# Kernel optimization log

Measured on AMD Instinct MI355X. Metric: run time of the kernel, lower is better.

## Reference

```python
import jax, jax.numpy as jnp
import numpy as np

NUM_EXPERTS = 8
HIDDEN = 2048
INTER = 4096
TOKENS = 8192  # divisible by NUM_EXPERTS


def setup_inputs() -> dict:
    key = jax.random.key(0)
    k1, k2, k3 = jax.random.split(key, 3)
    hidden_states = jax.random.normal(k1, (TOKENS, HIDDEN), dtype=jnp.float32)
    gate_up_proj = jax.random.normal(k2, (NUM_EXPERTS, HIDDEN, 2 * INTER), dtype=jnp.float32) * 0.02
    down_proj = jax.random.normal(k3, (NUM_EXPERTS, INTER, HIDDEN), dtype=jnp.float32) * 0.02
    return {"hidden_states": hidden_states, "gate_up_proj": gate_up_proj, "down_proj": down_proj}


def reference(hidden_states, gate_up_proj, down_proj):
    E, H = gate_up_proj.shape[0], gate_up_proj.shape[1]
    x = hidden_states.reshape(E, -1, H)                      # (E, T/E, H)
    gate_up = jnp.einsum('eth,ehf->etf', x, gate_up_proj)    # (E, T/E, 2I)
    gate, up = jnp.split(gate_up, 2, axis=-1)
    acted = up * jax.nn.silu(gate)                           # (E, T/E, I)
    out = jnp.einsum('eti,eih->eth', acted, down_proj)       # (E, T/E, H)
    return out.reshape(-1, H)
```

## Files before the change

kernel.cpp:

```cpp
#include <hip/hip_runtime.h>


#define E_   8
#define H_   2048
#define I_   4096
#define T_   8192
#define TPE  1024

typedef __bf16 bf16x8 __attribute__((ext_vector_type(8)));
typedef float  f32x4  __attribute__((ext_vector_type(4)));

__device__ __forceinline__ unsigned short f2bf(float f) {
  union { float f; unsigned int u; } v; v.f = f;
  unsigned int u = v.u;
  u += 0x7FFFu + ((u >> 16) & 1u);
  return (unsigned short)(u >> 16);
}

__device__ __forceinline__ void async16(const void* g, void* l) {
  __builtin_amdgcn_global_load_lds(
      (__attribute__((address_space(1))) void*)(g),
      (__attribute__((address_space(3))) void*)(l), 16, 0, 0);
}

#define SB0()      __builtin_amdgcn_sched_barrier(0)
#define BAR()      __builtin_amdgcn_s_barrier()
#define WAITLGKM() asm volatile("s_waitcnt lgkmcnt(0)" ::: "memory")
#define WAITVM(n)  asm volatile("s_waitcnt vmcnt(" #n ")" ::: "memory")

__global__ void convert_bf16(const float* __restrict__ src,
                             unsigned short* __restrict__ dst, long n) {
  long i = ((long)blockIdx.x * blockDim.x + threadIdx.x) * 4;
  const long stride = (long)gridDim.x * blockDim.x * 4;
  for (; i < n; i += stride) {
    const float4 v = *(const float4*)&src[i];
    ushort4 o;
    o.x = f2bf(v.x); o.y = f2bf(v.y); o.z = f2bf(v.z); o.w = f2bf(v.w);
    *(ushort4*)&dst[i] = o;
  }
}

template <int K, int NBN, int LDB, bool SILU>
__global__ __launch_bounds__(512, 2)
void gemm_fused(const unsigned short* __restrict__ Aall,
                const float* __restrict__ Ball,
                void* __restrict__ Cout,
                long sA, long sB, long sC) {
  extern __shared__ char smem[];
  constexpr int NT = K / 64;
  static_assert(NT % 2 == 0, "NT must be even for the x2 unroll");

  const int tid  = threadIdx.x;
  const int wave = tid >> 6;
  const int lane = tid & 63;
  const int lr   = lane & 15;
  const int lq   = lane >> 4;
  const int wid_m = wave >> 2;
  const int wid_n = wave & 3;

  const int nwg = gridDim.x;
  const int bid = blockIdx.x;
  const int wg  = (bid & 7) * (nwg >> 3) + (bid >> 3);
  const int mb  = wg & 3;
  const int tmp = wg >> 2;
  const int nb  = tmp % NBN;
  const int e   = tmp / NBN;

  const unsigned short* A = Aall + (long)e * sA + (long)(mb * 256) * K;
  const float*          B = Ball + (long)e * sB;

  const int stl  = tid >> 3;
  const int scol = ((tid & 7) ^ (stl & 7)) * 8;

  auto stageA = [&](int bi, int q, int kt) {
    const long col = (long)kt * 64 + scol;
    char* l0 = smem + bi * 32768 + q * 16384 + wave * 1024;
    async16(A + (long)(q * 64 + stl) * K + col,        l0);
    async16(A + (long)(128 + q * 64 + stl) * K + col,  l0 + 8192);
  };

  int cbase;
  if (SILU) {
    cbase = nb * 128 + (lane >> 5) * 64 + (lane & 15) * 4
          + (((lane >> 4) & 1) ? I_ : 0);
  } else {
    cbase = nb * 256 + lane * 4;
  }
  const float* Bq = B + cbase;

  f32x4 bvA[8], bvB[8];

  auto LOADB = [&](auto& bv, int kt) {
    const long kbase = (long)kt * 64 + wave * 8;
#pragma unroll
    for (int i = 0; i < 8; ++i)
      bv[i] = *(const f32x4*)&Bq[(kbase + i) * (long)LDB];
  };
  auto WRITEB = [&](int bo, auto& bv) {
    char* LBw = smem + 65536 + bo * 32768 + ((wave ^ (lane & 7)) * 16);
#pragma unroll
    for (int j = 0; j < 4; ++j) {
      bf16x8 pk;
#pragma unroll
      for (int i = 0; i < 8; ++i) pk[i] = (__bf16)bv[i][j];
      *(bf16x8*)(LBw + (64 * j + lane) * 128) = pk;
    }
  };

  const int ax0 = ((0 + lq) ^ (lr & 7)) * 16;
  const int ax1 = ((4 + lq) ^ (lr & 7)) * 16;

  f32x4 acc[8][4];
#pragma unroll
  for (int m = 0; m < 8; ++m)
#pragma unroll
    for (int n = 0; n < 4; ++n) acc[m][n] = (f32x4)0.0f;

  const int t1p = (NT > 1) ? 1 : 0;
  LOADB(bvA, 0);
  stageA(0, 0, 0);
  stageA(0, 1, 0);
  SB0();
  WAITVM(4); SB0();
  WRITEB(0, bvA);
  WAITLGKM(); SB0();
  stageA(1, 0, t1p); SB0();
  LOADB(bvB, t1p); SB0();
  stageA(1, 1, t1p); SB0();
  WAITVM(12); SB0();
  BAR();

  auto body = [&](int t, auto& bvW, auto& bvL) {
    const int cur = t & 1;
    const int bo  = cur ^ 1;
    const char* LA = smem + cur * 32768;
    const char* LB = smem + 65536 + cur * 32768;
    const int t2v = (t + 2 < NT) ? t + 2 : NT - 1;

    bf16x8 a[4][2], b0[2][2], b1[2][2];

#pragma unroll
    for (int mf = 0; mf < 4; ++mf) {
      const int st = wid_m * 64 + mf * 16 + lr;
      a[mf][0] = *(const bf16x8*)(LA + st * 128 + ax0);
      a[mf][1] = *(const bf16x8*)(LA + st * 128 + ax1);
    }
#pragma unroll
    for (int nf = 0; nf < 2; ++nf) {
      const int st = wid_n * 32 + nf * 16 + lr;
      b0[nf][0] = *(const bf16x8*)(LB + st * 128 + ax0);
      b0[nf][1] = *(const bf16x8*)(LB + st * 128 + ax1);
    }
    SB0();
    BAR();
    WAITLGKM(); SB0();
    __builtin_amdgcn_s_setprio(1);
#pragma unroll
    for (int mf = 0; mf < 4; ++mf)
#pragma unroll
      for (int nf = 0; nf < 2; ++nf) {
        acc[mf][nf] = __builtin_amdgcn_mfma_f32_16x16x32_bf16(a[mf][0], b0[nf][0], acc[mf][nf], 0, 0, 0);
        acc[mf][nf] = __builtin_amdgcn_mfma_f32_16x16x32_bf16(a[mf][1], b0[nf][1], acc[mf][nf], 0, 0, 0);
      }
    __builtin_amdgcn_s_setprio(0);
    BAR();

#pragma unroll
    for (int nf = 0; nf < 2; ++nf) {
      const int st = 128 + wid_n * 32 + nf * 16 + lr;
      b1[nf][0] = *(const bf16x8*)(LB + st * 128 + ax0);
      b1[nf][1] = *(const bf16x8*)(LB + st * 128 + ax1);
    }
    stageA(cur, 0, t2v);
    SB0();
    BAR();
    WAITLGKM(); SB0();
    __builtin_amdgcn_s_setprio(1);
#pragma unroll
    for (int mf = 0; mf < 4; ++mf)
#pragma unroll
      for (int nf = 0; nf < 2; ++nf) {
        acc[mf][2 + nf] = __builtin_amdgcn_mfma_f32_16x16x32_bf16(a[mf][0], b1[nf][0], acc[mf][2 + nf], 0, 0, 0);
        acc[mf][2 + nf] = __builtin_amdgcn_mfma_f32_16x16x32_bf16(a[mf][1], b1[nf][1], acc[mf][2 + nf], 0, 0, 0);
      }
    __builtin_amdgcn_s_setprio(0);
    BAR();

#pragma unroll
    for (int mf = 0; mf < 4; ++mf) {
      const int st = 128 + wid_m * 64 + mf * 16 + lr;
      a[mf][0] = *(const bf16x8*)(LA + st * 128 + ax0);
      a[mf][1] = *(const bf16x8*)(LA + st * 128 + ax1);
    }
    SB0();
    WAITVM(4); SB0();
    WRITEB(bo, bvW);
    LOADB(bvL, t2v);
    SB0();
    BAR();
    WAITLGKM(); SB0();
    __builtin_amdgcn_s_setprio(1);
#pragma unroll
    for (int mf = 0; mf < 4; ++mf)
#pragma unroll
      for (int nf = 0; nf < 2; ++nf) {
        acc[4 + mf][2 + nf] = __builtin_amdgcn_mfma_f32_16x16x32_bf16(a[mf][0], b1[nf][0], acc[4 + mf][2 + nf], 0, 0, 0);
        acc[4 + mf][2 + nf] = __builtin_amdgcn_mfma_f32_16x16x32_bf16(a[mf][1], b1[nf][1], acc[4 + mf][2 + nf], 0, 0, 0);
      }
    __builtin_amdgcn_s_setprio(0);
    BAR();

    stageA(cur, 1, t2v);
    SB0();
    WAITVM(12); SB0();
    BAR();
    __builtin_amdgcn_s_setprio(1);
#pragma unroll
    for (int mf = 0; mf < 4; ++mf)
#pragma unroll
      for (int nf = 0; nf < 2; ++nf) {
        acc[4 + mf][nf] = __builtin_amdgcn_mfma_f32_16x16x32_bf16(a[mf][0], b0[nf][0], acc[4 + mf][nf], 0, 0, 0);
        acc[4 + mf][nf] = __builtin_amdgcn_mfma_f32_16x16x32_bf16(a[mf][1], b0[nf][1], acc[4 + mf][nf], 0, 0, 0);
      }
    __builtin_amdgcn_s_setprio(0);
    BAR();
  };

#pragma unroll 1
  for (int tt = 0; tt < NT; tt += 2) {
    body(tt,     bvB, bvA);
    body(tt + 1, bvA, bvB);
  }

  WAITVM(0);

  if (SILU) {
    unsigned short* Cc = (unsigned short*)Cout + (long)e * sC;
#pragma unroll
    for (int mf = 0; mf < 8; ++mf)
#pragma unroll
      for (int p = 0; p < 2; ++p)
#pragma unroll
        for (int rr = 0; rr < 4; ++rr) {
          const int row = mb * 256 + wid_m * 128 + mf * 16 + lq * 4 + rr;
          const int col = nb * 128 + (wid_n & 1) * 64 + lr * 4
                        + 2 * p + (wid_n >> 1);
          const float g = acc[mf][p * 2][rr];
          const float u = acc[mf][p * 2 + 1][rr];
          Cc[(long)row * I_ + col] = f2bf(u * (g / (1.0f + __expf(-g))));
        }
  } else {
    float* Cc = (float*)Cout + (long)e * sC;
#pragma unroll
    for (int mf = 0; mf < 8; ++mf)
#pragma unroll
      for (int q = 0; q < 4; ++q)
#pragma unroll
        for (int rr = 0; rr < 4; ++rr) {
          const int row = mb * 256 + wid_m * 128 + mf * 16 + lq * 4 + rr;
          const int lp  = (wid_n & 1) * 32 + (q & 1) * 16 + lr;
          const int col = nb * 256 + lp * 4 + (q >> 1) * 2 + (wid_n >> 1);
          Cc[(long)row * H_ + col] = acc[mf][q][rr];
        }
  }
}

extern "C" void kernel_launch(void* const* d_in, const int* in_sizes, int n_in,
                              void* d_out, int out_size, void* d_ws, size_t ws_size,
                              hipStream_t stream) {
  const float* hs = (const float*)d_in[0];
  const float* w1 = (const float*)d_in[1];
  const float* w2 = (const float*)d_in[2];
  float* out = (float*)d_out;
  char* ws = (char*)d_ws;

  const long HB_B  = (long)T_ * H_ * 2;
  const long ACT_B = (long)T_ * I_ * 2;
  if (ws_size < (size_t)(HB_B + ACT_B)) return;

  unsigned short* hiddenB = (unsigned short*)(ws);
  unsigned short* acted   = (unsigned short*)(ws + HB_B);

  hipLaunchKernelGGL(convert_bf16, dim3(2048), dim3(256), 0, stream,
                     hs, hiddenB, (long)T_ * H_);

  hipLaunchKernelGGL((gemm_fused<H_, 32, 2 * I_, true>),
                     dim3(1024), dim3(512), 131072, stream,
                     hiddenB, w1, acted,
                     (long)TPE * H_, (long)H_ * 2 * I_, (long)TPE * I_);

  hipLaunchKernelGGL((gemm_fused<I_, 8, H_, false>),
                     dim3(256), dim3(512), 131072, stream,
                     acted, w2, out,
                     (long)TPE * I_, (long)I_ * H_, (long)TPE * H_);
}
```

Measured before the change: 595.3 us.

## Interleave B loads/writes across MFMA phases and stage epilogue through LDS

Measured after the change: 1.796 ms. 3.02x slower.

```diff
diff --git a/kernel.cpp b/kernel.cpp
--- a/kernel.cpp
+++ b/kernel.cpp
@@ -90,21 +90,18 @@
 
   f32x4 bvA[8], bvB[8];
 
-  auto LOADB = [&](auto& bv, int kt) {
-    const long kbase = (long)kt * 64 + wave * 8;
-#pragma unroll
-    for (int i = 0; i < 8; ++i)
-      bv[i] = *(const f32x4*)&Bq[(kbase + i) * (long)LDB];
+  auto LOADB4 = [&](auto& bv, int kt, int h) {
+    const long kbase = (long)kt * 64 + wave * 8 + h * 4;
+#pragma unroll
+    for (int i = 0; i < 4; ++i)
+      bv[4 * h + i] = *(const f32x4*)&Bq[(kbase + i) * (long)LDB];
   };
-  auto WRITEB = [&](int bo, auto& bv) {
+  auto WRITEB1 = [&](int bo, auto& bv, int j) {
     char* LBw = smem + 65536 + bo * 32768 + ((wave ^ (lane & 7)) * 16);
-#pragma unroll
-    for (int j = 0; j < 4; ++j) {
-      bf16x8 pk;
-#pragma unroll
-      for (int i = 0; i < 8; ++i) pk[i] = (__bf16)bv[i][j];
-      *(bf16x8*)(LBw + (64 * j + lane) * 128) = pk;
-    }
+    bf16x8 pk;
+#pragma unroll
+    for (int i = 0; i < 8; ++i) pk[i] = (__bf16)bv[i][j];
+    *(bf16x8*)(LBw + (64 * j + lane) * 128) = pk;
   };
 
   const int ax0 = ((0 + lq) ^ (lr & 7)) * 16;
@@ -117,17 +114,17 @@
     for (int n = 0; n < 4; ++n) acc[m][n] = (f32x4)0.0f;
 
   const int t1p = (NT > 1) ? 1 : 0;
-  LOADB(bvA, 0);
-  stageA(0, 0, 0);
-  stageA(0, 1, 0);
+  LOADB4(bvA, 0, 0); LOADB4(bvA, 0, 1);
+  stageA(0, 0, 0); stageA(0, 1, 0);
   SB0();
   WAITVM(4); SB0();
-  WRITEB(0, bvA);
+  WRITEB1(0, bvA, 0); WRITEB1(0, bvA, 1);
+  WRITEB1(0, bvA, 2); WRITEB1(0, bvA, 3);
+  LOADB4(bvB, t1p, 0); LOADB4(bvB, t1p, 1);
+  stageA(1, 0, t1p); stageA(1, 1, t1p);
+  SB0();
+  WAITVM(12); SB0();
   WAITLGKM(); SB0();
-  stageA(1, 0, t1p); SB0();
-  LOADB(bvB, t1p); SB0();
-  stageA(1, 1, t1p); SB0();
-  WAITVM(12); SB0();
   BAR();
 
   auto body = [&](int t, auto& bvW, auto& bvL) {
@@ -139,6 +136,8 @@
 
     bf16x8 a[4][2], b0[2][2], b1[2][2];
 
+    WAITVM(4); SB0();
+    WRITEB1(bo, bvW, 0);
 #pragma unroll
     for (int mf = 0; mf < 4; ++mf) {
       const int st = wid_m * 64 + mf * 16 + lr;
@@ -151,6 +150,7 @@
       b0[nf][0] = *(const bf16x8*)(LB + st * 128 + ax0);
       b0[nf][1] = *(const bf16x8*)(LB + st * 128 + ax1);
     }
+    LOADB4(bvL, t2v, 0);
     SB0();
     BAR();
     WAITLGKM(); SB0();
@@ -165,6 +165,7 @@
     __builtin_amdgcn_s_setprio(0);
     BAR();
 
+    WRITEB1(bo, bvW, 1);
 #pragma unroll
     for (int nf = 0; nf < 2; ++nf) {
       const int st = 128 + wid_n * 32 + nf * 16 + lr;
@@ -172,6 +173,7 @@
       b1[nf][1] = *(const bf16x8*)(LB + st * 128 + ax1);
     }
     stageA(cur, 0, t2v);
+    LOADB4(bvL, t2v, 1);
     SB0();
     BAR();
     WAITLGKM(); SB0();
@@ -186,16 +188,14 @@
     __builtin_amdgcn_s_setprio(0);
     BAR();
 
+    WRITEB1(bo, bvW, 2);
 #pragma unroll
     for (int mf = 0; mf < 4; ++mf) {
       const int st = 128 + wid_m * 64 + mf * 16 + lr;
       a[mf][0] = *(const bf16x8*)(LA + st * 128 + ax0);
       a[mf][1] = *(const bf16x8*)(LA + st * 128 + ax1);
     }
-    SB0();
-    WAITVM(4); SB0();
-    WRITEB(bo, bvW);
-    LOADB(bvL, t2v);
+    stageA(cur, 1, t2v);
     SB0();
     BAR();
     WAITLGKM(); SB0();
@@ -210,10 +210,11 @@
     __builtin_amdgcn_s_setprio(0);
     BAR();
 
-    stageA(cur, 1, t2v);
+    WRITEB1(bo, bvW, 3);
     SB0();
     WAITVM(12); SB0();
     BAR();
+    WAITLGKM(); SB0();
     __builtin_amdgcn_s_setprio(1);
 #pragma unroll
     for (int mf = 0; mf < 4; ++mf)
@@ -236,32 +237,55 @@
 
   if (SILU) {
     unsigned short* Cc = (unsigned short*)Cout + (long)e * sC;
+    BAR();
 #pragma unroll
     for (int mf = 0; mf < 8; ++mf)
 #pragma unroll
       for (int p = 0; p < 2; ++p)
 #pragma unroll
         for (int rr = 0; rr < 4; ++rr) {
-          const int row = mb * 256 + wid_m * 128 + mf * 16 + lq * 4 + rr;
-          const int col = nb * 128 + (wid_n & 1) * 64 + lr * 4
-                        + 2 * p + (wid_n >> 1);
+          const int row = wid_m * 128 + mf * 16 + lq * 4 + rr;
+          const int col = (wid_n & 1) * 64 + lr * 4 + 2 * p + (wid_n >> 1);
           const float g = acc[mf][p * 2][rr];
           const float u = acc[mf][p * 2 + 1][rr];
-          Cc[(long)row * I_ + col] = f2bf(u * (g / (1.0f + __expf(-g))));
+          *(unsigned short*)(smem + ((long)row * 128 + col) * 2) =
+              f2bf(u * (g / (1.0f + __expf(-g))));
         }
+    BAR();
+#pragma unroll
+    for (int pass = 0; pass < 8; ++pass) {
+      const int row = pass * 32 + (tid >> 4);
+      const int c8  = (tid & 15) * 8;
+      const f32x4 v = *(const f32x4*)(smem + ((long)row * 128 + c8) * 2);
+      *(f32x4*)((char*)&Cc[(long)(mb * 256 + row) * I_ + nb * 128 + c8]) = v;
+    }
   } else {
     float* Cc = (float*)Cout + (long)e * sC;
-#pragma unroll
-    for (int mf = 0; mf < 8; ++mf)
-#pragma unroll
-      for (int q = 0; q < 4; ++q)
-#pragma unroll
-        for (int rr = 0; rr < 4; ++rr) {
-          const int row = mb * 256 + wid_m * 128 + mf * 16 + lq * 4 + rr;
-          const int lp  = (wid_n & 1) * 32 + (q & 1) * 16 + lr;
-          const int col = nb * 256 + lp * 4 + (q >> 1) * 2 + (wid_n >> 1);
-          Cc[(long)row * H_ + col] = acc[mf][q][rr];
-        }
+#pragma unroll 1
+    for (int h = 0; h < 2; ++h) {
+      BAR();
+      if (wid_m == h) {
+#pragma unroll
+        for (int mf = 0; mf < 8; ++mf)
+#pragma unroll
+          for (int q = 0; q < 4; ++q)
+#pragma unroll
+            for (int rr = 0; rr < 4; ++rr) {
+              const int row = mf * 16 + lq * 4 + rr;
+              const int lp  = (wid_n & 1) * 32 + (q & 1) * 16 + lr;
+              const int col = lp * 4 + (q >> 1) * 2 + (wid_n >> 1);
+              *(float*)(smem + ((long)row * 256 + col) * 4) = acc[mf][q][rr];
+            }
+      }
+      BAR();
+#pragma unroll
+      for (int pass = 0; pass < 16; ++pass) {
+        const int row = pass * 8 + (tid >> 6);
+        const int c4  = (tid & 63) * 4;
+        const f32x4 v = *(const f32x4*)(smem + ((long)row * 256 + c4) * 4);
+        *(f32x4*)&Cc[(long)(mb * 256 + h * 128 + row) * H_ + nb * 256 + c4] = v;
+      }
+    }
   }
 }
 
```
